# Optimization experiments

Measured on AMD Instinct MI355X. Metric: run time of the kernel, lower is better.

Reference implementation:

```python
import jax, jax.numpy as jnp
import numpy as np

E = 8        # num_local_experts
D = 1024     # d_model
F = 4096     # d_ff
B = 2        # leading (ep/group) dim
T = E * 2048 # dim 1: E chunks of capacity 2048


def setup_inputs() -> dict:
    key = jax.random.key(0)
    ks = jax.random.split(key, 3)
    x = jax.random.normal(ks[0], (B, T, D), dtype=jnp.float32)
    # per-expert FFN params (same init scale as torch Linear default-ish)
    w1 = jax.random.normal(ks[1], (E, D, F), dtype=jnp.float32) * (1.0 / np.sqrt(D))
    b1 = jnp.zeros((E, F), dtype=jnp.float32)
    w2 = jax.random.normal(ks[2], (E, F, D), dtype=jnp.float32) * (1.0 / np.sqrt(F))
    b2 = jnp.zeros((E, D), dtype=jnp.float32)
    return {"x": x, "w1": w1, "b1": b1, "w2": w2, "b2": b2}


def reference(x, w1, b1, w2, b2):
    # torch: inputs.chunk(E, dim=1) -> per-expert FFN -> cat(dim=1)
    # Equivalent batched grouped-GEMM: reshape dim 1 into [E, C].
    b, t, d = x.shape
    c = t // E                                # capacity per expert
    xr = x.reshape(b, E, c, d)                # [B, E, C, D]
    h = jnp.einsum('becd,edf->becf', xr, w1) + b1[None, :, None, :]
    h = jax.nn.gelu(h, approximate=False)     # torch nn.GELU default (erf)
    out = jnp.einsum('becf,efd->becd', h, w2) + b2[None, :, None, :]
    return out.reshape(b, t, d)               # cat along dim=1
```

## Files before the change

### kernel.cpp

```cpp
#include <hip/hip_runtime.h>
#include <math.h>

typedef __bf16 bf16x8 __attribute__((ext_vector_type(8)));
typedef float f32x4 __attribute__((ext_vector_type(4)));

#define BM 128
#define BN 128
#define BK 64

__device__ __forceinline__ unsigned short f2bf(float f) {
    union { float f; unsigned u; } x; x.f = f;
    unsigned r = x.u + 0x7FFFu + ((x.u >> 16) & 1u);
    return (unsigned short)(r >> 16);
}

__device__ __forceinline__ float fast_gelu(float h) {
    const float z  = __builtin_fabsf(h) * 0.70710678118654752f;
    const float t  = __builtin_amdgcn_rcpf(__builtin_fmaf(0.3275911f, z, 1.0f));
    float p = 1.061405429f;
    p = __builtin_fmaf(p, t, -1.453152027f);
    p = __builtin_fmaf(p, t,  1.421413741f);
    p = __builtin_fmaf(p, t, -0.284496736f);
    p = __builtin_fmaf(p, t,  0.254829592f);
    const float ez = __builtin_amdgcn_exp2f(-z * z * 1.4426950408889634f);
    float erfz = __builtin_fmaf(-p * t, ez, 1.0f);
    erfz = (h < 0.0f) ? -erfz : erfz;
    return 0.5f * h * (1.0f + erfz);
}

#define GLOAD_LDS16(GP, LP)                                                      \
    __builtin_amdgcn_global_load_lds(                                            \
        (const __attribute__((address_space(1))) unsigned int*)(GP),             \
        (__attribute__((address_space(3))) unsigned int*)(LP), 16, 0, 0)

template <bool GELU, bool OUT_F32>
__global__ __launch_bounds__(256) void gemm_bt(
    const unsigned short* __restrict__ A,
    const unsigned short* __restrict__ Bt,
    const float* __restrict__ bias,
    void* __restrict__ Cv,
    int N, int K, int groupStart, int eStride, int groupPitch)
{
    __shared__ __attribute__((aligned(16))) unsigned short As[BM * BK];
    __shared__ __attribute__((aligned(16))) unsigned short Bs[BN * BK];

    const int tid  = threadIdx.x;
    const int lane = tid & 63;
    const int w    = tid >> 6;
    const int wm   = w & 1;
    const int wn   = w >> 1;

    const int rowBase = blockIdx.y * BM;
    const int colBase = blockIdx.x * BN;
    const int e = (groupStart + (int)(blockIdx.y >> 4) * eStride) & 7;

    const int swzChunk = ((lane & 7) ^ (lane >> 3)) * 8;
    const unsigned short* Ag = A + (size_t)(rowBase + w * 8 + (lane >> 3)) * K + swzChunk;
    const unsigned short* Bg = Bt + (size_t)e * N * K
                              + (size_t)(colBase + w * 8 + (lane >> 3)) * K + swzChunk;

    f32x4 acc[4][4];
    #pragma unroll
    for (int i = 0; i < 4; ++i)
        #pragma unroll
        for (int j = 0; j < 4; ++j)
            acc[i][j] = (f32x4){0.f, 0.f, 0.f, 0.f};

    const int lr = lane & 15;
    const int q  = lane >> 4;

    for (int kt = 0; kt < K; kt += BK) {
        #pragma unroll
        for (int p = 0; p < 4; ++p) {
            GLOAD_LDS16(Ag + (size_t)p * 32 * K + kt, &As[p * 2048 + w * 512]);
            GLOAD_LDS16(Bg + (size_t)p * 32 * K + kt, &Bs[p * 2048 + w * 512]);
        }
        asm volatile("s_waitcnt vmcnt(0)" ::: "memory");
        __syncthreads();

        #pragma unroll
        for (int kb = 0; kb < 2; ++kb) {
            const int pc = ((kb * 4 + q) ^ (lr & 7)) * 8;
            bf16x8 af[4], bfrag[4];
            #pragma unroll
            for (int i = 0; i < 4; ++i)
                af[i] = *(const bf16x8*)&As[(wm * 64 + i * 16 + lr) * BK + pc];
            #pragma unroll
            for (int j = 0; j < 4; ++j)
                bfrag[j] = *(const bf16x8*)&Bs[(wn * 64 + j * 16 + lr) * BK + pc];
            #pragma unroll
            for (int i = 0; i < 4; ++i)
                #pragma unroll
                for (int j = 0; j < 4; ++j)
                    acc[i][j] = __builtin_amdgcn_mfma_f32_16x16x32_bf16(
                        af[i], bfrag[j], acc[i][j], 0, 0, 0);
        }
        __syncthreads();
    }

    const float* be = bias + (size_t)e * N;
    float bj[4];
    #pragma unroll
    for (int j = 0; j < 4; ++j)
        bj[j] = be[colBase + wn * 64 + j * 16 + lr];

    #pragma unroll
    for (int i = 0; i < 4; ++i) {
        #pragma unroll
        for (int r = 0; r < 4; ++r) {
            const int rowLocal = rowBase + wm * 64 + i * 16 + q * 4 + r;
            const int rowG = (rowLocal >> 11) * groupPitch + (rowLocal & 2047);
            #pragma unroll
            for (int j = 0; j < 4; ++j) {
                const int col = colBase + wn * 64 + j * 16 + lr;
                float v = acc[i][j][r] + bj[j];
                if (GELU) v = fast_gelu(v);
                if (OUT_F32)
                    ((float*)Cv)[(size_t)rowG * N + col] = v;
                else
                    ((unsigned short*)Cv)[(size_t)rowG * N + col] = f2bf(v);
            }
        }
    }
}

__global__ __launch_bounds__(256) void transpose_cvt(
    const float* __restrict__ W, unsigned short* __restrict__ Wt,
    int R, int C)
{
    __shared__ unsigned short t64[64][68];
    const int t = threadIdx.x;
    const int r0 = blockIdx.y * 64, c0 = blockIdx.x * 64;
    const float* Wp = W + (size_t)blockIdx.z * R * C;
    unsigned short* Wtp = Wt + (size_t)blockIdx.z * R * C;

    #pragma unroll
    for (int p = 0; p < 4; ++p) {
        const int row = p * 16 + (t >> 4);
        const int c4  = (t & 15) * 4;
        float4 v = *(const float4*)&Wp[(size_t)(r0 + row) * C + c0 + c4];
        t64[row][c4 + 0] = f2bf(v.x);
        t64[row][c4 + 1] = f2bf(v.y);
        t64[row][c4 + 2] = f2bf(v.z);
        t64[row][c4 + 3] = f2bf(v.w);
    }
    __syncthreads();
    #pragma unroll
    for (int p = 0; p < 4; ++p) {
        const int oc = p * 16 + (t >> 4);
        const int r4 = (t & 15) * 4;
        ushort4 o;
        o.x = t64[r4 + 0][oc];
        o.y = t64[r4 + 1][oc];
        o.z = t64[r4 + 2][oc];
        o.w = t64[r4 + 3][oc];
        *(ushort4*)&Wtp[(size_t)(c0 + oc) * R + r0 + r4] = o;
    }
}

__global__ __launch_bounds__(256) void cvt_f32_bf16(
    const float* __restrict__ in, unsigned short* __restrict__ out, long long n)
{
    long long i = ((long long)blockIdx.x * 256 + threadIdx.x) * 4;
    if (i < n) {
        float4 v = *(const float4*)&in[i];
        ushort4 o;
        o.x = f2bf(v.x); o.y = f2bf(v.y); o.z = f2bf(v.z); o.w = f2bf(v.w);
        *(ushort4*)&out[i] = o;
    }
}

extern "C" void kernel_launch(void* const* d_in, const int* in_sizes, int n_in,
                              void* d_out, int out_size, void* d_ws, size_t ws_size,
                              hipStream_t stream) {
    const float* x  = (const float*)d_in[0];
    const float* w1 = (const float*)d_in[1];
    const float* b1 = (const float*)d_in[2];
    const float* w2 = (const float*)d_in[3];
    const float* b2 = (const float*)d_in[4];
    float* out = (float*)d_out;
    unsigned short* ws = (unsigned short*)d_ws;

    const int E = 8, D = 1024, F = 4096, Bdim = 2, Cap = 2048;
    const int T = E * Cap;
    const size_t xbE = (size_t)Bdim * T * D;
    const size_t wE  = (size_t)E * D * F;
    const size_t gE  = (size_t)Cap * F;

    dim3 blk(256);
    const size_t fullBytes = (xbE + 2 * wE + gE) * 2;

    if (ws_size >= fullBytes) {
        unsigned short* xb  = ws;
        unsigned short* w1t = ws + xbE;
        unsigned short* w2t = ws + xbE + wE;
        unsigned short* H   = ws + xbE + 2 * wE;
        int gpc = (int)((ws_size / 2 - (xbE + 2 * wE)) / gE);
        if (gpc > 16) gpc = 16;
        if (gpc < 1)  gpc = 1;

        cvt_f32_bf16<<<(unsigned)((xbE / 4 + 255) / 256), blk, 0, stream>>>(x, xb, (long long)xbE);
        transpose_cvt<<<dim3(F / 64, D / 64, E), blk, 0, stream>>>(w1, w1t, D, F);
        transpose_cvt<<<dim3(D / 64, F / 64, E), blk, 0, stream>>>(w2, w2t, F, D);

        for (int g0 = 0; g0 < Bdim * E; g0 += gpc) {
            const int ng = (g0 + gpc <= Bdim * E) ? gpc : (Bdim * E - g0);
            gemm_bt<true, false><<<dim3(F / BN, ng * 16), blk, 0, stream>>>(
                xb + (size_t)g0 * Cap * D, w1t, b1, H, F, D, g0, 1, 2048);
            gemm_bt<false, true><<<dim3(D / BN, ng * 16), blk, 0, stream>>>(
                H, w2t, b2, out + (size_t)g0 * Cap * D, D, F, g0, 1, 2048);
        }
    } else {
        unsigned short* w1t = ws;
        unsigned short* w2t = w1t + (size_t)F * D;
        unsigned short* xb  = w2t + (size_t)D * F;
        unsigned short* H   = xb + 2 * (size_t)Cap * D;

        for (int e = 0; e < E; ++e) {
            transpose_cvt<<<dim3(F / 64, D / 64, 1), blk, 0, stream>>>(
                w1 + (size_t)e * D * F, w1t, D, F);
            transpose_cvt<<<dim3(D / 64, F / 64, 1), blk, 0, stream>>>(
                w2 + (size_t)e * F * D, w2t, F, D);
            for (int b = 0; b < Bdim; ++b)
                cvt_f32_bf16<<<(unsigned)(((size_t)Cap * D / 4 + 255) / 256), blk, 0, stream>>>(
                    x + ((size_t)b * T + (size_t)e * Cap) * D,
                    xb + (size_t)b * Cap * D, (long long)Cap * D);
            gemm_bt<true, false><<<dim3(F / BN, 32), blk, 0, stream>>>(
                xb, w1t, b1, H, F, D, e, 0, 2048);
            gemm_bt<false, true><<<dim3(D / BN, 32), blk, 0, stream>>>(
                H, w2t, b2, out + (size_t)e * Cap * D, D, F, e, 0, T);
        }
    }
}
```

Baseline: 1.097 ms.

## Use 256x256 tiles with 512 threads and double-buffered LDS pipeline

Grows the GEMM block tile to 256x256 with 8 waves per block and double-buffers the A/B LDS tiles. Each K-step is split into four quadrant phases, and the async global-to-LDS loads for the next tile are interleaved with the MFMA work on the current one. Barriers with partial vmcnt waits and s_setprio are used to hide memory latency. This targets load stalls and the low arithmetic intensity of 128x128 tiles, at the cost of much higher register and LDS use per block and fewer blocks for the D=1024 second GEMM.

```diff
diff --git a/kernel.cpp b/kernel.cpp
--- a/kernel.cpp
+++ b/kernel.cpp
@@ -4,8 +4,8 @@
 typedef __bf16 bf16x8 __attribute__((ext_vector_type(8)));
 typedef float f32x4 __attribute__((ext_vector_type(4)));
 
-#define BM 128
-#define BN 128
+#define BM 256
+#define BN 256
 #define BK 64
 
 __device__ __forceinline__ unsigned short f2bf(float f) {
@@ -33,16 +33,69 @@
         (const __attribute__((address_space(1))) unsigned int*)(GP),             \
         (__attribute__((address_space(3))) unsigned int*)(LP), 16, 0, 0)
 
+
+#define STAGE_A(sl, h, kto) do {                                                      \
+    GLOAD_LDS16(Ag + (size_t)((h) * 128 + 0) * K + (kto), &As[sl][((h) * 128 + stRow + 0) * BK]); \
+    GLOAD_LDS16(Ag + (size_t)((h) * 128 + 8) * K + (kto), &As[sl][((h) * 128 + stRow + 8) * BK]); \
+} while (0)
+
+#define STAGE_B(sl, h, kto) do {                                                      \
+    GLOAD_LDS16(Bg + (size_t)((h) * 128 + 0) * K + (kto), &Bs[sl][((h) * 128 + stRow + 0) * BK]); \
+    GLOAD_LDS16(Bg + (size_t)((h) * 128 + 8) * K + (kto), &Bs[sl][((h) * 128 + stRow + 8) * BK]); \
+} while (0)
+
+#define LDA(sl, rh) do {                                                              \
+    const unsigned short* _pa = &As[sl][((rh) * 128 + wm * 64 + lr) * BK];            \
+    _Pragma("unroll") for (int _i = 0; _i < 4; ++_i) {                                \
+        af[_i][0] = *(const bf16x8*)&_pa[_i * 16 * BK + pc0];                         \
+        af[_i][1] = *(const bf16x8*)&_pa[_i * 16 * BK + pc1];                         \
+    }                                                                                 \
+} while (0)
+
+#define LDB(sl, ch) do {                                                              \
+    const unsigned short* _pb = &Bs[sl][((ch) * 128 + wn * 32 + lr) * BK];            \
+    _Pragma("unroll") for (int _j = 0; _j < 2; ++_j) {                                \
+        bfr[_j][0] = *(const bf16x8*)&_pb[_j * 16 * BK + pc0];                        \
+        bfr[_j][1] = *(const bf16x8*)&_pb[_j * 16 * BK + pc1];                        \
+    }                                                                                 \
+} while (0)
+
+#define MM(rh, ch) do {                                                               \
+    _Pragma("unroll") for (int _i = 0; _i < 4; ++_i)                                  \
+    _Pragma("unroll") for (int _j = 0; _j < 2; ++_j) {                                \
+        acc[(rh) * 4 + _i][(ch) * 2 + _j] = __builtin_amdgcn_mfma_f32_16x16x32_bf16(  \
+            af[_i][0], bfr[_j][0], acc[(rh) * 4 + _i][(ch) * 2 + _j], 0, 0, 0);       \
+        acc[(rh) * 4 + _i][(ch) * 2 + _j] = __builtin_amdgcn_mfma_f32_16x16x32_bf16(  \
+            af[_i][1], bfr[_j][1], acc[(rh) * 4 + _i][(ch) * 2 + _j], 0, 0, 0);       \
+    }                                                                                 \
+} while (0)
+
+#define MIDBAR() do {                                                                 \
+    __builtin_amdgcn_s_barrier();                                                     \
+    asm volatile("s_waitcnt lgkmcnt(0)" ::: "memory");                                \
+    __builtin_amdgcn_sched_barrier(0);                                                \
+} while (0)
+
+#define ENDBAR_W() do {                                                               \
+    asm volatile("s_waitcnt vmcnt(4)" ::: "memory");                                  \
+    __builtin_amdgcn_s_barrier();                                                     \
+} while (0)
+
+#define ENDBAR_N() do {                                                               \
+    asm volatile("" ::: "memory");                                                    \
+    __builtin_amdgcn_s_barrier();                                                     \
+} while (0)
+
 template <bool GELU, bool OUT_F32>
-__global__ __launch_bounds__(256) void gemm_bt(
+__global__ __launch_bounds__(512, 2) void gemm_bt(
     const unsigned short* __restrict__ A,
     const unsigned short* __restrict__ Bt,
     const float* __restrict__ bias,
     void* __restrict__ Cv,
     int N, int K, int groupStart, int eStride, int groupPitch)
 {
-    __shared__ __attribute__((aligned(16))) unsigned short As[BM * BK];
-    __shared__ __attribute__((aligned(16))) unsigned short Bs[BN * BK];
+    __shared__ __attribute__((aligned(16))) unsigned short As[2][BM * BK];
+    __shared__ __attribute__((aligned(16))) unsigned short Bs[2][BN * BK];
 
     const int tid  = threadIdx.x;
     const int lane = tid & 63;
@@ -52,74 +105,97 @@
 
     const int rowBase = blockIdx.y * BM;
     const int colBase = blockIdx.x * BN;
-    const int e = (groupStart + (int)(blockIdx.y >> 4) * eStride) & 7;
-
-    const int swzChunk = ((lane & 7) ^ (lane >> 3)) * 8;
-    const unsigned short* Ag = A + (size_t)(rowBase + w * 8 + (lane >> 3)) * K + swzChunk;
+    const int e = (groupStart + (int)(blockIdx.y >> 3) * eStride) & 7;
+
+    const int sRow   = w * 16 + (lane >> 3);
+    const int sChunk = ((lane & 7) ^ (lane >> 3)) * 8;
+    const unsigned short* Ag = A + (size_t)(rowBase + sRow) * K + sChunk;
     const unsigned short* Bg = Bt + (size_t)e * N * K
-                              + (size_t)(colBase + w * 8 + (lane >> 3)) * K + swzChunk;
-
-    f32x4 acc[4][4];
-    #pragma unroll
-    for (int i = 0; i < 4; ++i)
+                              + (size_t)(colBase + sRow) * K + sChunk;
+    const int stRow = w * 16;
+
+    const int lr  = lane & 15;
+    const int q   = lane >> 4;
+    const int pc0 = ((0 + q) ^ (lr & 7)) * 8;
+    const int pc1 = ((4 + q) ^ (lr & 7)) * 8;
+
+    f32x4 acc[8][4];
+    #pragma unroll
+    for (int i = 0; i < 8; ++i)
         #pragma unroll
         for (int j = 0; j < 4; ++j)
             acc[i][j] = (f32x4){0.f, 0.f, 0.f, 0.f};
 
-    const int lr = lane & 15;
-    const int q  = lane >> 4;
-
-    for (int kt = 0; kt < K; kt += BK) {
+    bf16x8 af[4][2];
+    bf16x8 bfr[2][2];
+
+    const int NT = K / BK;
+
+    STAGE_A(0, 0, 0);
+    STAGE_B(0, 0, 0);
+    STAGE_B(0, 1, 0);
+    STAGE_A(0, 1, 0);
+    asm volatile("s_waitcnt vmcnt(4)" ::: "memory");
+    __builtin_amdgcn_s_barrier();
+
+    for (int t = 0; t < NT; ++t) {
+        const int sl  = t & 1;
+        const int ns  = sl ^ 1;
+        const int ktn = (t + 1 == NT) ? 0 : (t + 1) * BK;
+
+        LDA(sl, 0); LDB(sl, 0);
+        STAGE_A(ns, 0, ktn);
+        MIDBAR();
+        __builtin_amdgcn_s_setprio(1); MM(0, 0); __builtin_amdgcn_s_setprio(0);
+        ENDBAR_W();
+
+        LDB(sl, 1);
+        STAGE_B(ns, 0, ktn);
+        MIDBAR();
+        __builtin_amdgcn_s_setprio(1); MM(0, 1); __builtin_amdgcn_s_setprio(0);
+        ENDBAR_W();
+
+        LDA(sl, 1);
+        STAGE_B(ns, 1, ktn);
+        MIDBAR();
+        __builtin_amdgcn_s_setprio(1); MM(1, 1); __builtin_amdgcn_s_setprio(0);
+        ENDBAR_N();
+
+        LDB(sl, 0);
+        STAGE_A(ns, 1, ktn);
+        MIDBAR();
+        __builtin_amdgcn_s_setprio(1); MM(1, 0); __builtin_amdgcn_s_setprio(0);
+        ENDBAR_W();
+    }
+    asm volatile("s_waitcnt vmcnt(0)" ::: "memory");
+
+    const float* be = bias + (size_t)e * N;
+    float bj[2][2];
+    #pragma unroll
+    for (int ch = 0; ch < 2; ++ch)
         #pragma unroll
-        for (int p = 0; p < 4; ++p) {
-            GLOAD_LDS16(Ag + (size_t)p * 32 * K + kt, &As[p * 2048 + w * 512]);
-            GLOAD_LDS16(Bg + (size_t)p * 32 * K + kt, &Bs[p * 2048 + w * 512]);
-        }
-        asm volatile("s_waitcnt vmcnt(0)" ::: "memory");
-        __syncthreads();
-
+        for (int j = 0; j < 2; ++j)
+            bj[ch][j] = be[colBase + ch * 128 + wn * 32 + j * 16 + lr];
+
+    #pragma unroll
+    for (int rh = 0; rh < 2; ++rh)
+    #pragma unroll
+    for (int i = 0; i < 4; ++i)
+    #pragma unroll
+    for (int r = 0; r < 4; ++r) {
+        const int rowLocal = rowBase + rh * 128 + wm * 64 + i * 16 + q * 4 + r;
+        const int rowG = (rowLocal >> 11) * groupPitch + (rowLocal & 2047);
         #pragma unroll
-        for (int kb = 0; kb < 2; ++kb) {
-            const int pc = ((kb * 4 + q) ^ (lr & 7)) * 8;
-            bf16x8 af[4], bfrag[4];
-            #pragma unroll
-            for (int i = 0; i < 4; ++i)
-                af[i] = *(const bf16x8*)&As[(wm * 64 + i * 16 + lr) * BK + pc];
-            #pragma unroll
-            for (int j = 0; j < 4; ++j)
-                bfrag[j] = *(const bf16x8*)&Bs[(wn * 64 + j * 16 + lr) * BK + pc];
-            #pragma unroll
-            for (int i = 0; i < 4; ++i)
-                #pragma unroll
-                for (int j = 0; j < 4; ++j)
-                    acc[i][j] = __builtin_amdgcn_mfma_f32_16x16x32_bf16(
-                        af[i], bfrag[j], acc[i][j], 0, 0, 0);
-        }
-        __syncthreads();
-    }
-
-    const float* be = bias + (size_t)e * N;
-    float bj[4];
-    #pragma unroll
-    for (int j = 0; j < 4; ++j)
-        bj[j] = be[colBase + wn * 64 + j * 16 + lr];
-
-    #pragma unroll
-    for (int i = 0; i < 4; ++i) {
+        for (int ch = 0; ch < 2; ++ch)
         #pragma unroll
-        for (int r = 0; r < 4; ++r) {
-            const int rowLocal = rowBase + wm * 64 + i * 16 + q * 4 + r;
-            const int rowG = (rowLocal >> 11) * groupPitch + (rowLocal & 2047);
-            #pragma unroll
-            for (int j = 0; j < 4; ++j) {
-                const int col = colBase + wn * 64 + j * 16 + lr;
-                float v = acc[i][j][r] + bj[j];
-                if (GELU) v = fast_gelu(v);
-                if (OUT_F32)
-                    ((float*)Cv)[(size_t)rowG * N + col] = v;
-                else
-                    ((unsigned short*)Cv)[(size_t)rowG * N + col] = f2bf(v);
-            }
+        for (int j = 0; j < 2; ++j) {
+            const int col = colBase + ch * 128 + wn * 32 + j * 16 + lr;
+            float v = acc[rh * 4 + i][ch * 2 + j][r] + bj[ch][j];
+            if (GELU) v = fast_gelu(v);
+            if (OUT_F32)
+                ((float*)Cv)[(size_t)rowG * N + col] = v;
+            else
+                ((unsigned short*)Cv)[(size_t)rowG * N + col] = f2bf(v);
         }
     }
 }
@@ -188,6 +264,7 @@
     const size_t gE  = (size_t)Cap * F;
 
     dim3 blk(256);
+    dim3 gblk(512);
     const size_t fullBytes = (xbE + 2 * wE + gE) * 2;
 
     if (ws_size >= fullBytes) {
@@ -205,9 +282,9 @@
 
         for (int g0 = 0; g0 < Bdim * E; g0 += gpc) {
             const int ng = (g0 + gpc <= Bdim * E) ? gpc : (Bdim * E - g0);
-            gemm_bt<true, false><<<dim3(F / BN, ng * 16), blk, 0, stream>>>(
+            gemm_bt<true, false><<<dim3(F / BN, ng * 8), gblk, 0, stream>>>(
                 xb + (size_t)g0 * Cap * D, w1t, b1, H, F, D, g0, 1, 2048);
-            gemm_bt<false, true><<<dim3(D / BN, ng * 16), blk, 0, stream>>>(
+            gemm_bt<false, true><<<dim3(D / BN, ng * 8), gblk, 0, stream>>>(
                 H, w2t, b2, out + (size_t)g0 * Cap * D, D, F, g0, 1, 2048);
         }
     } else {
@@ -225,9 +302,9 @@
                 cvt_f32_bf16<<<(unsigned)(((size_t)Cap * D / 4 + 255) / 256), blk, 0, stream>>>(
                     x + ((size_t)b * T + (size_t)e * Cap) * D,
                     xb + (size_t)b * Cap * D, (long long)Cap * D);
-            gemm_bt<true, false><<<dim3(F / BN, 32), blk, 0, stream>>>(
+            gemm_bt<true, false><<<dim3(F / BN, 16), gblk, 0, stream>>>(
                 xb, w1t, b1, H, F, D, e, 0, 2048);
-            gemm_bt<false, true><<<dim3(D / BN, 32), blk, 0, stream>>>(
+            gemm_bt<false, true><<<dim3(D / BN, 16), gblk, 0, stream>>>(
                 H, w2t, b2, out + (size_t)e * Cap * D, D, F, e, 0, T);
         }
     }
```

Result: no change. 1.085 ms (-1.1%).

## Double-buffer LDS with 256x128 tiles, 8 waves, and XCD-aware block remap

Applied to the files above, without the earlier changes.

The GEMM kernel moves to 512-thread blocks computing 256x128 tiles with BK=32. LDS is now double-buffered, so global-to-LDS loads for the next K step are issued while MFMAs run on the current one, using fine-grained barriers and s_setprio. Block IDs are remapped across the 8 XCDs to improve L2 locality, and the LDS swizzle is changed to match the new tile shape. The aim is to hide global-load latency and raise MFMA utilisation. The cost is a more fragile vmcnt/barrier schedule and more accumulator register pressure per wave.

```diff
diff --git a/kernel.cpp b/kernel.cpp
--- a/kernel.cpp
+++ b/kernel.cpp
@@ -4,9 +4,9 @@
 typedef __bf16 bf16x8 __attribute__((ext_vector_type(8)));
 typedef float f32x4 __attribute__((ext_vector_type(4)));
 
-#define BM 128
+#define BM 256
 #define BN 128
-#define BK 64
+#define BK 32
 
 __device__ __forceinline__ unsigned short f2bf(float f) {
     union { float f; unsigned u; } x; x.f = f;
@@ -33,16 +33,41 @@
         (const __attribute__((address_space(1))) unsigned int*)(GP),             \
         (__attribute__((address_space(3))) unsigned int*)(LP), 16, 0, 0)
 
+
+#define STAGE_A(sl, h, kto)                                                      \
+    GLOAD_LDS16(Ag + (size_t)((h) * 128) * K + (kto), &As[sl][(h) * 128 * BK + aBase])
+#define STAGE_B(sl, kto)                                                         \
+    GLOAD_LDS16(Bg + (kto), &Bs[sl][aBase])
+
+#define LDA(sl, rh) do {                                                         \
+    const unsigned short* _pa = &As[sl][((rh) * 128 + wm * 64 + lr) * BK + pc];  \
+    _Pragma("unroll") for (int _i = 0; _i < 4; ++_i)                             \
+        af[_i] = *(const bf16x8*)&_pa[_i * 16 * BK];                             \
+} while (0)
+
+#define LDB(sl) do {                                                             \
+    const unsigned short* _pb = &Bs[sl][(wn * 32 + lr) * BK + pc];               \
+    _Pragma("unroll") for (int _j = 0; _j < 2; ++_j)                             \
+        bfr[_j] = *(const bf16x8*)&_pb[_j * 16 * BK];                            \
+} while (0)
+
+#define MM(rh) do {                                                              \
+    _Pragma("unroll") for (int _i = 0; _i < 4; ++_i)                             \
+    _Pragma("unroll") for (int _j = 0; _j < 2; ++_j)                             \
+        acc[(rh) * 4 + _i][_j] = __builtin_amdgcn_mfma_f32_16x16x32_bf16(        \
+            af[_i], bfr[_j], acc[(rh) * 4 + _i][_j], 0, 0, 0);                   \
+} while (0)
+
 template <bool GELU, bool OUT_F32>
-__global__ __launch_bounds__(256) void gemm_bt(
+__global__ __launch_bounds__(512, 4) void gemm_bt(
     const unsigned short* __restrict__ A,
     const unsigned short* __restrict__ Bt,
     const float* __restrict__ bias,
     void* __restrict__ Cv,
     int N, int K, int groupStart, int eStride, int groupPitch)
 {
-    __shared__ __attribute__((aligned(16))) unsigned short As[BM * BK];
-    __shared__ __attribute__((aligned(16))) unsigned short Bs[BN * BK];
+    __shared__ __attribute__((aligned(16))) unsigned short As[2][BM * BK];
+    __shared__ __attribute__((aligned(16))) unsigned short Bs[2][BN * BK];
 
     const int tid  = threadIdx.x;
     const int lane = tid & 63;
@@ -50,76 +75,94 @@
     const int wm   = w & 1;
     const int wn   = w >> 1;
 
-    const int rowBase = blockIdx.y * BM;
-    const int colBase = blockIdx.x * BN;
-    const int e = (groupStart + (int)(blockIdx.y >> 4) * eStride) & 7;
-
-    const int swzChunk = ((lane & 7) ^ (lane >> 3)) * 8;
-    const unsigned short* Ag = A + (size_t)(rowBase + w * 8 + (lane >> 3)) * K + swzChunk;
+    const int gx = (int)gridDim.x;
+    const unsigned total = gridDim.x * gridDim.y;
+    const unsigned orig  = blockIdx.y * gridDim.x + blockIdx.x;
+    const unsigned nid   = (orig & 7u) * (total >> 3) + (orig >> 3);
+    const int bx = (int)(nid % (unsigned)gx);
+    const int by = (int)(nid / (unsigned)gx);
+
+    const int rowBase = by * BM;
+    const int colBase = bx * BN;
+    const int e = (groupStart + (by >> 3) * eStride) & 7;
+
+    const int g = ((lane & 3) - ((lane >> 3) & 3)) & 3;
+    const unsigned short* Ag = A + (size_t)(rowBase + w * 16 + (lane >> 2)) * K + g * 8;
     const unsigned short* Bg = Bt + (size_t)e * N * K
-                              + (size_t)(colBase + w * 8 + (lane >> 3)) * K + swzChunk;
-
-    f32x4 acc[4][4];
-    #pragma unroll
-    for (int i = 0; i < 4; ++i)
-        #pragma unroll
-        for (int j = 0; j < 4; ++j)
-            acc[i][j] = (f32x4){0.f, 0.f, 0.f, 0.f};
+                              + (size_t)(colBase + w * 16 + (lane >> 2)) * K + g * 8;
+    const int aBase = w * 16 * BK;
 
     const int lr = lane & 15;
     const int q  = lane >> 4;
-
-    for (int kt = 0; kt < K; kt += BK) {
+    const int pc = ((q + (lr >> 1)) & 3) * 8;
+
+    f32x4 acc[8][2];
+    #pragma unroll
+    for (int i = 0; i < 8; ++i)
         #pragma unroll
-        for (int p = 0; p < 4; ++p) {
-            GLOAD_LDS16(Ag + (size_t)p * 32 * K + kt, &As[p * 2048 + w * 512]);
-            GLOAD_LDS16(Bg + (size_t)p * 32 * K + kt, &Bs[p * 2048 + w * 512]);
-        }
-        asm volatile("s_waitcnt vmcnt(0)" ::: "memory");
-        __syncthreads();
-
+        for (int j = 0; j < 2; ++j)
+            acc[i][j] = (f32x4){0.f, 0.f, 0.f, 0.f};
+
+    bf16x8 af[4], bfr[2];
+
+    const int NT = K / BK;
+
+    STAGE_A(0, 0, 0);
+    STAGE_B(0, 0);
+    STAGE_A(0, 1, 0);
+    asm volatile("s_waitcnt vmcnt(1)" ::: "memory");
+    __builtin_amdgcn_s_barrier();
+    asm volatile("" ::: "memory");
+
+    for (int t = 0; t < NT; ++t) {
+        const int sl  = t & 1;
+        const int ns  = sl ^ 1;
+        const int ktn = (t + 1 < NT) ? (t + 1) * BK : 0;
+
+        LDB(sl); LDA(sl, 0);
+        STAGE_A(ns, 0, ktn);
+        STAGE_B(ns, ktn);
+        __builtin_amdgcn_s_barrier();
+        asm volatile("s_waitcnt lgkmcnt(0)");
+        __builtin_amdgcn_s_setprio(1); MM(0); __builtin_amdgcn_s_setprio(0);
+        asm volatile("s_waitcnt vmcnt(2)" ::: "memory");
+        __builtin_amdgcn_s_barrier();
+        asm volatile("" ::: "memory");
+
+        LDA(sl, 1);
+        STAGE_A(ns, 1, ktn);
+        __builtin_amdgcn_s_barrier();
+        asm volatile("s_waitcnt lgkmcnt(0)");
+        __builtin_amdgcn_s_setprio(1); MM(1); __builtin_amdgcn_s_setprio(0);
+        asm volatile("s_waitcnt vmcnt(1)" ::: "memory");
+        __builtin_amdgcn_s_barrier();
+        asm volatile("" ::: "memory");
+    }
+    asm volatile("s_waitcnt vmcnt(0)" ::: "memory");
+
+    const float* be = bias + (size_t)e * N;
+    float bj[2];
+    #pragma unroll
+    for (int j = 0; j < 2; ++j)
+        bj[j] = be[colBase + wn * 32 + j * 16 + lr];
+
+    #pragma unroll
+    for (int rh = 0; rh < 2; ++rh)
+    #pragma unroll
+    for (int i = 0; i < 4; ++i)
+    #pragma unroll
+    for (int r = 0; r < 4; ++r) {
+        const int rowLocal = rowBase + rh * 128 + wm * 64 + i * 16 + q * 4 + r;
+        const int rowG = (rowLocal >> 11) * groupPitch + (rowLocal & 2047);
         #pragma unroll
-        for (int kb = 0; kb < 2; ++kb) {
-            const int pc = ((kb * 4 + q) ^ (lr & 7)) * 8;
-            bf16x8 af[4], bfrag[4];
-            #pragma unroll
-            for (int i = 0; i < 4; ++i)
-                af[i] = *(const bf16x8*)&As[(wm * 64 + i * 16 + lr) * BK + pc];
-            #pragma unroll
-            for (int j = 0; j < 4; ++j)
-                bfrag[j] = *(const bf16x8*)&Bs[(wn * 64 + j * 16 + lr) * BK + pc];
-            #pragma unroll
-            for (int i = 0; i < 4; ++i)
-                #pragma unroll
-                for (int j = 0; j < 4; ++j)
-                    acc[i][j] = __builtin_amdgcn_mfma_f32_16x16x32_bf16(
-                        af[i], bfrag[j], acc[i][j], 0, 0, 0);
-        }
-        __syncthreads();
-    }
-
-    const float* be = bias + (size_t)e * N;
-    float bj[4];
-    #pragma unroll
-    for (int j = 0; j < 4; ++j)
-        bj[j] = be[colBase + wn * 64 + j * 16 + lr];
-
-    #pragma unroll
-    for (int i = 0; i < 4; ++i) {
-        #pragma unroll
-        for (int r = 0; r < 4; ++r) {
-            const int rowLocal = rowBase + wm * 64 + i * 16 + q * 4 + r;
-            const int rowG = (rowLocal >> 11) * groupPitch + (rowLocal & 2047);
-            #pragma unroll
-            for (int j = 0; j < 4; ++j) {
-                const int col = colBase + wn * 64 + j * 16 + lr;
-                float v = acc[i][j][r] + bj[j];
-                if (GELU) v = fast_gelu(v);
-                if (OUT_F32)
-                    ((float*)Cv)[(size_t)rowG * N + col] = v;
-                else
-                    ((unsigned short*)Cv)[(size_t)rowG * N + col] = f2bf(v);
-            }
+        for (int j = 0; j < 2; ++j) {
+            const int col = colBase + wn * 32 + j * 16 + lr;
+            float v = acc[rh * 4 + i][j][r] + bj[j];
+            if (GELU) v = fast_gelu(v);
+            if (OUT_F32)
+                ((float*)Cv)[(size_t)rowG * N + col] = v;
+            else
+                ((unsigned short*)Cv)[(size_t)rowG * N + col] = f2bf(v);
         }
     }
 }
@@ -188,6 +231,7 @@
     const size_t gE  = (size_t)Cap * F;
 
     dim3 blk(256);
+    dim3 gblk(512);
     const size_t fullBytes = (xbE + 2 * wE + gE) * 2;
 
     if (ws_size >= fullBytes) {
@@ -205,9 +249,9 @@
 
         for (int g0 = 0; g0 < Bdim * E; g0 += gpc) {
             const int ng = (g0 + gpc <= Bdim * E) ? gpc : (Bdim * E - g0);
-            gemm_bt<true, false><<<dim3(F / BN, ng * 16), blk, 0, stream>>>(
+            gemm_bt<true, false><<<dim3(F / BN, ng * 8), gblk, 0, stream>>>(
                 xb + (size_t)g0 * Cap * D, w1t, b1, H, F, D, g0, 1, 2048);
-            gemm_bt<false, true><<<dim3(D / BN, ng * 16), blk, 0, stream>>>(
+            gemm_bt<false, true><<<dim3(D / BN, ng * 8), gblk, 0, stream>>>(
                 H, w2t, b2, out + (size_t)g0 * Cap * D, D, F, g0, 1, 2048);
         }
     } else {
@@ -225,9 +269,9 @@
                 cvt_f32_bf16<<<(unsigned)(((size_t)Cap * D / 4 + 255) / 256), blk, 0, stream>>>(
                     x + ((size_t)b * T + (size_t)e * Cap) * D,
                     xb + (size_t)b * Cap * D, (long long)Cap * D);
-            gemm_bt<true, false><<<dim3(F / BN, 32), blk, 0, stream>>>(
+            gemm_bt<true, false><<<dim3(F / BN, 16), gblk, 0, stream>>>(
                 xb, w1t, b1, H, F, D, e, 0, 2048);
-            gemm_bt<false, true><<<dim3(D / BN, 32), blk, 0, stream>>>(
+            gemm_bt<false, true><<<dim3(D / BN, 16), gblk, 0, stream>>>(
                 H, w2t, b2, out + (size_t)e * Cap * D, D, F, e, 0, T);
         }
     }
```

New measurement: 1.062 ms. -3.2%, faster.
